# Performance work log

Measured on AMD Instinct MI355X. Metric: run time of the kernel, lower is better.

The kernel has to match this reference:

```python
import jax, jax.numpy as jnp
import numpy as np

B, E, H, N = 16, 1024, 16, 2048
Eh = E // H   # head dim = 64
BH = B * H    # 256


def setup_inputs() -> dict:
    key = jax.random.key(0)
    ks = jax.random.split(key, 12)
    query = jax.random.normal(ks[0], (B, E), jnp.float32)
    key_in = jax.random.normal(ks[1], (B, E), jnp.float32)
    value = jax.random.normal(ks[2], (B, E), jnp.float32)
    # State as it would look in steady state: a_sum ~ O(N) positive,
    # q_mem stores already-scaled queries (small), k/v unit-ish scale.
    a_sum_mem = float(N) * (0.9 + 0.2 * jax.random.uniform(ks[3], (BH, N - 1), jnp.float32))
    av_mem = (0.1 * float(N)) * jax.random.normal(ks[4], (BH, N - 1, Eh), jnp.float32)
    q_mem = 0.06 * jax.random.normal(ks[5], (BH, N, Eh), jnp.float32)
    k_t_mem = 0.5 * jax.random.normal(ks[6], (BH, Eh, N), jnp.float32)
    v_mem = 0.5 * jax.random.normal(ks[7], (BH, N, Eh), jnp.float32)
    in_proj_weight = 0.02 * jax.random.normal(ks[8], (3 * E, E), jnp.float32)
    in_proj_bias = jnp.zeros((3 * E,), jnp.float32)
    out_proj_weight = 0.02 * jax.random.normal(ks[9], (E, E), jnp.float32)
    out_proj_bias = jnp.zeros((E,), jnp.float32)
    return dict(query=query, key=key_in, value=value,
                a_sum_mem=a_sum_mem, av_mem=av_mem, q_mem=q_mem,
                k_t_mem=k_t_mem, v_mem=v_mem,
                in_proj_weight=in_proj_weight, in_proj_bias=in_proj_bias,
                out_proj_weight=out_proj_weight, out_proj_bias=out_proj_bias)


def _sdpa_step(a_sum_mem, av_mem, q_mem, k_t_mem, v_mem, q_step, k_step, v_step):
    # Faithful port of _scaled_dot_product_attention_step.
    q_step = q_step / jnp.sqrt(jnp.float32(Eh))          # (BH, Eh)
    q_old = q_mem[:, 0]                                   # (BH, Eh)
    k_old = k_t_mem[:, :, 0]                              # (BH, Eh)
    q_sel = jnp.stack((q_old, q_step), axis=1)            # (BH, 2, Eh)
    k_sel = jnp.stack((k_old, k_step), axis=2)            # (BH, Eh, 2)
    a_tb = jnp.exp(jnp.einsum('bte,bes->bts', q_sel, k_t_mem[:, :, 1:]))  # (BH, 2, N-1)
    a_lr = jnp.exp(jnp.einsum('bne,bet->bnt', q_mem[:, 1:, :], k_sel))    # (BH, N-1, 2)
    a_br = jnp.exp(jnp.sum(q_step * k_step, axis=1))      # (BH,)
    a_sum = jnp.concatenate(
        [a_sum_mem + a_lr[:, :, 1] - a_lr[:, :, 0],
         (a_tb[:, 1].sum(axis=1) + a_br)[:, None]], axis=1)               # (BH, N)
    av_top = (av_mem
              - a_lr[:, :, 0, None] * v_mem[:, 0][:, None, :]
              + a_lr[:, :, 1, None] * v_step[:, None, :])                 # (BH, N-1, Eh)
    av_bot = jnp.einsum('bs,bse->be', a_tb[:, 1], v_mem[:, 1:]) + a_br[:, None] * v_step
    av = jnp.concatenate([av_top, av_bot[:, None, :]], axis=1)            # (BH, N, Eh)
    out = av / a_sum[..., None]
    new_state = (a_sum[:, 1:], av[:, 1:],
                 jnp.concatenate([q_mem[:, 1:], q_step[:, None, :]], axis=1),
                 jnp.concatenate([k_t_mem[:, :, 1:], k_step[:, :, None]], axis=2),
                 jnp.concatenate([v_mem[:, 1:], v_step[:, None, :]], axis=1))
    return out, new_state


def reference(query, key, value, a_sum_mem, av_mem, q_mem, k_t_mem, v_mem,
              in_proj_weight, in_proj_bias, out_proj_weight, out_proj_bias):
    # Packed in-projection (q/k/v chunks of the packed weight).
    w_q, w_k, w_v = jnp.split(in_proj_weight, 3, axis=0)
    b_q, b_k, b_v = jnp.split(in_proj_bias, 3)
    q = (query @ w_q.T + b_q).reshape(BH, Eh)   # head split: (B, H*Eh) -> (B*H, Eh)
    k = (key @ w_k.T + b_k).reshape(BH, Eh)
    v = (value @ w_v.T + b_v).reshape(BH, Eh)
    attn, new_state = _sdpa_step(a_sum_mem, av_mem, q_mem, k_t_mem, v_mem, q, k, v)
    # (BH, N, Eh) -> (N, BH, Eh) -> (N, B, E), then output projection.
    attn = attn.transpose(1, 0, 2).reshape(N, B, E)
    out = attn @ out_proj_weight.T + out_proj_bias    # (N, B, E)
    return (out,) + new_state
```

## Files before the change

kernel.cpp:

```cpp
#include <hip/hip_runtime.h>
#include <hip/hip_bf16.h>

constexpr int kB  = 16;
constexpr int kE  = 1024;
constexpr int kH  = 16;
constexpr int kN  = 2048;
constexpr int kEh = 64;
constexpr int kBH = 256;
constexpr int kM  = kN * kB;

typedef __bf16 bf16x8 __attribute__((ext_vector_type(8)));
typedef float  f32x4  __attribute__((ext_vector_type(4)));

static __device__ __forceinline__ unsigned short bf16_bits(float f) {
  union { __hip_bfloat16 h; unsigned short u; } cv;
  cv.h = __float2bfloat16(f);
  return cv.u;
}

__global__ __launch_bounds__(256) void proj_kernel(
    const float* __restrict__ query, const float* __restrict__ key_in,
    const float* __restrict__ value, const float* __restrict__ W,
    const float* __restrict__ bias,
    float* __restrict__ q_step, float* __restrict__ k_step,
    float* __restrict__ v_step) {
  int j   = blockIdx.x;
  int mat = j >> 10;
  int col = j & 1023;
  const float* in = (mat == 0) ? query : ((mat == 1) ? key_in : value);
  const float* wrow = W + (size_t)j * kE;
  int tid = threadIdx.x;

  float4 w4 = reinterpret_cast<const float4*>(wrow)[tid];
  float part[16];
#pragma unroll
  for (int r = 0; r < 16; ++r) {
    float4 in4 = reinterpret_cast<const float4*>(in + (size_t)r * kE)[tid];
    part[r] = w4.x * in4.x + w4.y * in4.y + w4.z * in4.z + w4.w * in4.w;
  }
#pragma unroll
  for (int r = 0; r < 16; ++r) {
    float v = part[r];
    for (int off = 32; off > 0; off >>= 1) v += __shfl_down(v, off, 64);
    part[r] = v;
  }
  __shared__ float red[4][16];
  int wave = threadIdx.x >> 6;
  int lane = threadIdx.x & 63;
  if (lane == 0) {
#pragma unroll
    for (int r = 0; r < 16; ++r) red[wave][r] = part[r];
  }
  __syncthreads();
  if (threadIdx.x < 16) {
    int r = threadIdx.x;
    float v = red[0][r] + red[1][r] + red[2][r] + red[3][r] + bias[j];
    int h = col >> 6, eh = col & 63;
    int bh = r * kH + h;
    if (mat == 0)      q_step[bh * kEh + eh] = v * 0.125f;
    else if (mat == 1) k_step[bh * kEh + eh] = v;
    else               v_step[bh * kEh + eh] = v;
  }
}

__global__ void wcvt_kernel(const float* __restrict__ w,
                            __hip_bfloat16* __restrict__ o, int n) {
  int i = blockIdx.x * blockDim.x + threadIdx.x;
  if (i < n) o[i] = __float2bfloat16(w[i]);
}

__global__ __launch_bounds__(256) void kt_kernel(
    const float* __restrict__ k_t_mem, const float* __restrict__ q_step,
    float* __restrict__ k_t_out, float* __restrict__ a_tb1,
    float* __restrict__ top_sum) {
  int b = blockIdx.x;
  int chunk = blockIdx.y;
  __shared__ float qs[64];
  if (threadIdx.x < 64) qs[threadIdx.x] = q_step[b * kEh + threadIdx.x];
  __syncthreads();

  int c4 = (chunk * 256 + threadIdx.x) * 4;
  bool last = (c4 + 4 >= kN);
  const float* src = k_t_mem + (size_t)b * kEh * kN;
  float* dst = k_t_out + (size_t)b * kEh * kN;

  f32x4 dot = {0.f, 0.f, 0.f, 0.f};
#pragma unroll 4
  for (int e = 0; e < 64; ++e) {
    float4 a = reinterpret_cast<const float4*>(src + (size_t)e * kN)[c4 >> 2];
    float s3 = last ? 0.f : src[(size_t)e * kN + c4 + 4];
    float4 sh = {a.y, a.z, a.w, s3};
    reinterpret_cast<float4*>(dst + (size_t)e * kN)[c4 >> 2] = sh;
    float q = qs[e];
    dot.x += q * sh.x;
    dot.y += q * sh.y;
    dot.z += q * sh.z;
    dot.w += q * sh.w;
  }
  float tx = __expf(dot.x);
  float ty = __expf(dot.y);
  float tz = __expf(dot.z);
  float tw = last ? 0.f : __expf(dot.w);

  float* tbrow = a_tb1 + (size_t)b * (kN - 1);
  tbrow[c4 + 0] = tx;
  tbrow[c4 + 1] = ty;
  tbrow[c4 + 2] = tz;
  if (!last) tbrow[c4 + 3] = tw;

  float s = tx + ty + tz + tw;
  for (int off = 32; off > 0; off >>= 1) s += __shfl_xor(s, off, 64);
  __shared__ float red[4];
  int wave = threadIdx.x >> 6, lane = threadIdx.x & 63;
  if (lane == 0) red[wave] = s;
  __syncthreads();
  if (threadIdx.x == 0)
    atomicAdd(&top_sum[b], red[0] + red[1] + red[2] + red[3]);
}

__global__ __launch_bounds__(256) void qav_kernel(
    const float* __restrict__ q_mem, const float* __restrict__ av_mem,
    const float* __restrict__ a_sum_mem, const float* __restrict__ k_t_mem,
    const float* __restrict__ v_mem, const float* __restrict__ k_step,
    const float* __restrict__ v_step, float* __restrict__ q_out,
    float* __restrict__ av_out, float* __restrict__ a_sum_out,
    __hip_bfloat16* __restrict__ attn) {
  int b = blockIdx.x;
  int chunk = blockIdx.y;
  int wave = threadIdx.x >> 6, lane = threadIdx.x & 63;
  int g = lane >> 4, c = lane & 15;
  int b_ = b >> 4, h = b & 15;

  float4 kst  = reinterpret_cast<const float4*>(k_step + (size_t)b * kEh)[c];
  float4 vst  = reinterpret_cast<const float4*>(v_step + (size_t)b * kEh)[c];
  float4 vold = reinterpret_cast<const float4*>(v_mem + (size_t)b * kN * kEh)[c];
  const float* kt0 = k_t_mem + (size_t)b * kEh * kN;
  float4 kold;
  kold.x = kt0[(size_t)(4 * c + 0) * kN];
  kold.y = kt0[(size_t)(4 * c + 1) * kN];
  kold.z = kt0[(size_t)(4 * c + 2) * kN];
  kold.w = kt0[(size_t)(4 * c + 3) * kN];

  unsigned short* attn_u = reinterpret_cast<unsigned short*>(attn);

  int jb = chunk * 64 + wave * 16;
#pragma unroll
  for (int it = 0; it < 4; ++it) {
    int j = jb + it * 4 + g;
    bool valid = (j <= kN - 2);
    int jc = valid ? j : (kN - 2);

    float4 q4 = reinterpret_cast<const float4*>(
        q_mem + ((size_t)b * kN + (jc + 1)) * kEh)[c];
    float p0 = q4.x * kold.x + q4.y * kold.y + q4.z * kold.z + q4.w * kold.w;
    float p1 = q4.x * kst.x + q4.y * kst.y + q4.z * kst.z + q4.w * kst.w;
#pragma unroll
    for (int off = 1; off < 16; off <<= 1) {
      p0 += __shfl_xor(p0, off, 64);
      p1 += __shfl_xor(p1, off, 64);
    }
    float a0 = __expf(p0);
    float a1 = __expf(p1);
    float asum = a_sum_mem[(size_t)b * (kN - 1) + jc] + a1 - a0;
    float4 av4 = reinterpret_cast<const float4*>(
        av_mem + ((size_t)b * (kN - 1) + jc) * kEh)[c];
    float4 avv;
    avv.x = av4.x - a0 * vold.x + a1 * vst.x;
    avv.y = av4.y - a0 * vold.y + a1 * vst.y;
    avv.z = av4.z - a0 * vold.z + a1 * vst.z;
    avv.w = av4.w - a0 * vold.w + a1 * vst.w;

    if (valid) {
      reinterpret_cast<float4*>(q_out + ((size_t)b * kN + jc) * kEh)[c] = q4;
      float inv = 1.0f / asum;
      ushort4 pk;
      pk.x = bf16_bits(avv.x * inv);
      pk.y = bf16_bits(avv.y * inv);
      pk.z = bf16_bits(avv.z * inv);
      pk.w = bf16_bits(avv.w * inv);
      *reinterpret_cast<ushort4*>(
          attn_u + ((size_t)jc * kB + b_) * kE + h * kEh + c * 4) = pk;
      if (j >= 1) {
        reinterpret_cast<float4*>(
            av_out + ((size_t)b * (kN - 1) + (jc - 1)) * kEh)[c] = avv;
        if (c == 0) a_sum_out[(size_t)b * (kN - 1) + (jc - 1)] = asum;
      }
    }
  }
}

__global__ __launch_bounds__(256) void v_kernel(
    const float* __restrict__ v_mem, const float* __restrict__ a_tb1,
    float* __restrict__ v_out, float* __restrict__ av_last) {
  int b = blockIdx.x;
  int chunk = blockIdx.y;
  int wave = threadIdx.x >> 6, lane = threadIdx.x & 63;
  int g = lane >> 4, c = lane & 15;
  const float* vsrc = v_mem + (size_t)b * kN * kEh;
  float* vdst = v_out + (size_t)b * kN * kEh;
  const float* tb = a_tb1 + (size_t)b * (kN - 1);

  f32x4 acc = {0.f, 0.f, 0.f, 0.f};
  int sbase = chunk * 256 + wave * 64;
#pragma unroll 4
  for (int it = 0; it < 16; ++it) {
    int s = sbase + it * 4 + g;
    bool valid = (s <= kN - 2);
    int sc = valid ? s : (kN - 2);
    float t = valid ? tb[sc] : 0.f;
    float4 vv = reinterpret_cast<const float4*>(vsrc + (size_t)(sc + 1) * kEh)[c];
    acc.x += t * vv.x;
    acc.y += t * vv.y;
    acc.z += t * vv.z;
    acc.w += t * vv.w;
    if (valid)
      reinterpret_cast<float4*>(vdst + (size_t)sc * kEh)[c] = vv;
  }
#pragma unroll
  for (int off = 16; off <= 32; off <<= 1) {
    acc.x += __shfl_xor(acc.x, off, 64);
    acc.y += __shfl_xor(acc.y, off, 64);
    acc.z += __shfl_xor(acc.z, off, 64);
    acc.w += __shfl_xor(acc.w, off, 64);
  }
  __shared__ f32x4 red[4][16];
  if (g == 0) red[wave][c] = acc;
  __syncthreads();
  if (threadIdx.x < 16) {
    f32x4 a0 = red[0][threadIdx.x], a1 = red[1][threadIdx.x];
    f32x4 a2 = red[2][threadIdx.x], a3 = red[3][threadIdx.x];
    float* dst = av_last + (size_t)b * kEh + threadIdx.x * 4;
    atomicAdd(dst + 0, a0.x + a1.x + a2.x + a3.x);
    atomicAdd(dst + 1, a0.y + a1.y + a2.y + a3.y);
    atomicAdd(dst + 2, a0.z + a1.z + a2.z + a3.z);
    atomicAdd(dst + 3, a0.w + a1.w + a2.w + a3.w);
  }
}

__global__ __launch_bounds__(64) void final_kernel(
    const float* __restrict__ q_step, const float* __restrict__ k_step,
    const float* __restrict__ v_step, const float* __restrict__ top_sum,
    const float* __restrict__ av_last_in, float* __restrict__ q_out,
    float* __restrict__ k_t_out, float* __restrict__ v_out,
    float* __restrict__ a_sum_out, float* __restrict__ av_out,
    __hip_bfloat16* __restrict__ attn) {
  int b = blockIdx.x;
  int lane = threadIdx.x;
  int b_ = b >> 4, h = b & 15;
  float qs = q_step[b * kEh + lane];
  float ks = k_step[b * kEh + lane];
  float vs = v_step[b * kEh + lane];
  float p = qs * ks;
  for (int off = 32; off > 0; off >>= 1) p += __shfl_xor(p, off, 64);
  float abr = __expf(p);
  float asum = top_sum[b] + abr;
  float avl = av_last_in[b * kEh + lane] + abr * vs;
  attn[((size_t)(kN - 1) * kB + b_) * kE + h * kEh + lane] =
      __float2bfloat16(avl / asum);
  if (lane == 0) a_sum_out[(size_t)b * (kN - 1) + (kN - 2)] = asum;
  av_out[((size_t)b * (kN - 1) + (kN - 2)) * kEh + lane] = avl;
  q_out[((size_t)b * kN + (kN - 1)) * kEh + lane] = qs;
  k_t_out[(size_t)b * kEh * kN + (size_t)lane * kN + (kN - 1)] = ks;
  v_out[((size_t)b * kN + (kN - 1)) * kEh + lane] = vs;
}

#define BM 128
#define BN 128
#define BK 64

__global__ __launch_bounds__(256) void gemm_kernel(
    const __bf16* __restrict__ A, const __bf16* __restrict__ Bw,
    const float* __restrict__ bias, float* __restrict__ C,
    int M, int Ncols, int K) {
  __shared__ __bf16 lA[BM * BK];
  __shared__ __bf16 lB[BN * BK];
  int tid = threadIdx.x;
  int m0 = blockIdx.x * BM;
  int n0 = blockIdx.y * BN;
  int wave = tid >> 6;
  int lane = tid & 63;
  int wm = (wave & 1) * 64;
  int wn = (wave >> 1) * 64;

  f32x4 zero = {0.f, 0.f, 0.f, 0.f};
  f32x4 acc[4][4];
#pragma unroll
  for (int i = 0; i < 4; ++i)
#pragma unroll
    for (int j = 0; j < 4; ++j) acc[i][j] = zero;

  int quad = lane >> 4;
  int mrow = lane & 15;

  for (int k0 = 0; k0 < K; k0 += BK) {
#pragma unroll
    for (int r = 0; r < 4; ++r) {
      int off = r * 4096 + tid * 16;
      int row = off >> 7;
      int col8 = (off >> 4) & 7;
      const __bf16* ga = A + ((size_t)(m0 + row) * K + k0 + col8 * 8);
      const __bf16* gb = Bw + ((size_t)(n0 + row) * K + k0 + col8 * 8);
      __builtin_amdgcn_global_load_lds(
          (const __attribute__((address_space(1))) void*)ga,
          (__attribute__((address_space(3))) void*)((char*)lA + off), 16, 0, 0);
      __builtin_amdgcn_global_load_lds(
          (const __attribute__((address_space(1))) void*)gb,
          (__attribute__((address_space(3))) void*)((char*)lB + off), 16, 0, 0);
    }
    __syncthreads();

#pragma unroll
    for (int kk = 0; kk < 2; ++kk) {
      bf16x8 af[4], bfr[4];
#pragma unroll
      for (int i = 0; i < 4; ++i) {
        af[i]  = *(const bf16x8*)(&lA[(wm + i * 16 + mrow) * BK + kk * 32 + quad * 8]);
        bfr[i] = *(const bf16x8*)(&lB[(wn + i * 16 + mrow) * BK + kk * 32 + quad * 8]);
      }
#pragma unroll
      for (int i = 0; i < 4; ++i)
#pragma unroll
        for (int j = 0; j < 4; ++j)
          acc[i][j] = __builtin_amdgcn_mfma_f32_16x16x32_bf16(
              af[i], bfr[j], acc[i][j], 0, 0, 0);
    }
    __syncthreads();
  }

  int colq = lane & 15;
  int rowq = lane >> 4;
#pragma unroll
  for (int i = 0; i < 4; ++i) {
#pragma unroll
    for (int j = 0; j < 4; ++j) {
      int col = n0 + wn + j * 16 + colq;
      float bv = bias[col];
      size_t base = (size_t)(m0 + wm + i * 16 + rowq * 4) * Ncols + col;
#pragma unroll
      for (int r = 0; r < 4; ++r) {
        C[base + (size_t)r * Ncols] = acc[i][j][r] + bv;
      }
    }
  }
}

extern "C" void kernel_launch(void* const* d_in, const int* in_sizes, int n_in,
                              void* d_out, int out_size, void* d_ws,
                              size_t ws_size, hipStream_t stream) {
  const float* query          = (const float*)d_in[0];
  const float* key_in         = (const float*)d_in[1];
  const float* value          = (const float*)d_in[2];
  const float* a_sum_mem      = (const float*)d_in[3];
  const float* av_mem         = (const float*)d_in[4];
  const float* q_mem          = (const float*)d_in[5];
  const float* k_t_mem        = (const float*)d_in[6];
  const float* v_mem          = (const float*)d_in[7];
  const float* in_proj_weight = (const float*)d_in[8];
  const float* in_proj_bias   = (const float*)d_in[9];
  const float* out_proj_weight= (const float*)d_in[10];
  const float* out_proj_bias  = (const float*)d_in[11];

  float* out       = (float*)d_out;
  float* a_sum_out = out + (size_t)kN * kB * kE;
  float* av_out    = a_sum_out + (size_t)kBH * (kN - 1);
  float* q_out     = av_out + (size_t)kBH * (kN - 1) * kEh;
  float* k_t_out   = q_out + (size_t)kBH * kN * kEh;
  float* v_out     = k_t_out + (size_t)kBH * kEh * kN;

  char* ws = (char*)d_ws;
  float* q_step  = (float*)ws;
  float* k_step  = q_step + 16384;
  float* v_step  = k_step + 16384;
  float* top_sum = v_step + 16384;
  float* av_last = top_sum + 256;
  float* a_tb1   = av_last + 16384;
  __hip_bfloat16* wo_bf   = (__hip_bfloat16*)(ws + 2359296);
  __hip_bfloat16* attn_bf = (__hip_bfloat16*)(ws + 4456448);

  hipMemsetAsync(ws + 196608, 0, 66560, stream);

  proj_kernel<<<3 * kE, 256, 0, stream>>>(query, key_in, value, in_proj_weight,
                                          in_proj_bias, q_step, k_step, v_step);
  wcvt_kernel<<<(kE * kE) / 256, 256, 0, stream>>>(out_proj_weight, wo_bf,
                                                   kE * kE);
  kt_kernel<<<dim3(kBH, 2), 256, 0, stream>>>(k_t_mem, q_step, k_t_out, a_tb1,
                                              top_sum);
  qav_kernel<<<dim3(kBH, 32), 256, 0, stream>>>(q_mem, av_mem, a_sum_mem,
                                                k_t_mem, v_mem, k_step, v_step,
                                                q_out, av_out, a_sum_out,
                                                attn_bf);
  v_kernel<<<dim3(kBH, 8), 256, 0, stream>>>(v_mem, a_tb1, v_out, av_last);
  final_kernel<<<kBH, 64, 0, stream>>>(q_step, k_step, v_step, top_sum,
                                       av_last, q_out, k_t_out, v_out,
                                       a_sum_out, av_out, attn_bf);
  gemm_kernel<<<dim3(kM / BM, kE / BN), 256, 0, stream>>>(
      (const __bf16*)attn_bf, (const __bf16*)wo_bf, out_proj_bias, out, kM, kE,
      kE);
}
```

Before: 1.172 ms.

## Merge streaming kernels into one launch with nontemporal memory ops

Folds the weight-conversion kernel into the projection kernel as extra blocks. Merges the k_t shift, q/av update and v shift kernels into a single streaming kernel. The top-row exp weights now stay in shared memory instead of a global scratch buffer, and each k_t/v block covers 1024 columns. Nontemporal loads and stores are applied to the large streaming buffers and to the GEMM output, to cut launch count and cache pollution. The cost is fewer, larger k_t/v blocks with longer serial loops, which may lower parallelism for that part.

```diff
diff --git a/kernel.cpp b/kernel.cpp
--- a/kernel.cpp
+++ b/kernel.cpp
@@ -11,6 +11,7 @@
 
 typedef __bf16 bf16x8 __attribute__((ext_vector_type(8)));
 typedef float  f32x4  __attribute__((ext_vector_type(4)));
+typedef unsigned short u16x4 __attribute__((ext_vector_type(4)));
 
 static __device__ __forceinline__ unsigned short bf16_bits(float f) {
   union { __hip_bfloat16 h; unsigned short u; } cv;
@@ -18,18 +19,37 @@
   return cv.u;
 }
 
-__global__ __launch_bounds__(256) void proj_kernel(
+static __device__ __forceinline__ f32x4 nt_load4(const float* p) {
+  return __builtin_nontemporal_load(reinterpret_cast<const f32x4*>(p));
+}
+static __device__ __forceinline__ void nt_store4(float* p, f32x4 v) {
+  __builtin_nontemporal_store(v, reinterpret_cast<f32x4*>(p));
+}
+
+__global__ __launch_bounds__(256) void prep_kernel(
     const float* __restrict__ query, const float* __restrict__ key_in,
     const float* __restrict__ value, const float* __restrict__ W,
     const float* __restrict__ bias,
     float* __restrict__ q_step, float* __restrict__ k_step,
-    float* __restrict__ v_step) {
-  int j   = blockIdx.x;
+    float* __restrict__ v_step,
+    const float* __restrict__ wo, __hip_bfloat16* __restrict__ wo_bf) {
+  __shared__ float red[4][16];
+  int bid = blockIdx.x;
+  int tid = threadIdx.x;
+  if (bid >= 3072) {
+    int i4 = ((bid - 3072) * 256 + tid) * 4;
+    f32x4 w4 = nt_load4(wo + i4);
+    u16x4 o;
+    o[0] = bf16_bits(w4[0]); o[1] = bf16_bits(w4[1]);
+    o[2] = bf16_bits(w4[2]); o[3] = bf16_bits(w4[3]);
+    *reinterpret_cast<u16x4*>(reinterpret_cast<unsigned short*>(wo_bf) + i4) = o;
+    return;
+  }
+  int j   = bid;
   int mat = j >> 10;
   int col = j & 1023;
   const float* in = (mat == 0) ? query : ((mat == 1) ? key_in : value);
   const float* wrow = W + (size_t)j * kE;
-  int tid = threadIdx.x;
 
   float4 w4 = reinterpret_cast<const float4*>(wrow)[tid];
   float part[16];
@@ -44,16 +64,15 @@
     for (int off = 32; off > 0; off >>= 1) v += __shfl_down(v, off, 64);
     part[r] = v;
   }
-  __shared__ float red[4][16];
-  int wave = threadIdx.x >> 6;
-  int lane = threadIdx.x & 63;
+  int wave = tid >> 6;
+  int lane = tid & 63;
   if (lane == 0) {
 #pragma unroll
     for (int r = 0; r < 16; ++r) red[wave][r] = part[r];
   }
   __syncthreads();
-  if (threadIdx.x < 16) {
-    int r = threadIdx.x;
+  if (tid < 16) {
+    int r = tid;
     float v = red[0][r] + red[1][r] + red[2][r] + red[3][r] + bias[j];
     int h = col >> 6, eh = col & 63;
     int bh = r * kH + h;
@@ -63,23 +82,93 @@
   }
 }
 
-__global__ void wcvt_kernel(const float* __restrict__ w,
-                            __hip_bfloat16* __restrict__ o, int n) {
-  int i = blockIdx.x * blockDim.x + threadIdx.x;
-  if (i < n) o[i] = __float2bfloat16(w[i]);
-}
-
-__global__ __launch_bounds__(256) void kt_kernel(
-    const float* __restrict__ k_t_mem, const float* __restrict__ q_step,
-    float* __restrict__ k_t_out, float* __restrict__ a_tb1,
-    float* __restrict__ top_sum) {
-  int b = blockIdx.x;
-  int chunk = blockIdx.y;
+__global__ __launch_bounds__(256) void stream_kernel(
+    const float* __restrict__ q_mem, const float* __restrict__ av_mem,
+    const float* __restrict__ a_sum_mem, const float* __restrict__ k_t_mem,
+    const float* __restrict__ v_mem, const float* __restrict__ q_step,
+    const float* __restrict__ k_step, const float* __restrict__ v_step,
+    float* __restrict__ q_out, float* __restrict__ av_out,
+    float* __restrict__ a_sum_out, float* __restrict__ k_t_out,
+    float* __restrict__ v_out, float* __restrict__ top_sum,
+    float* __restrict__ av_last, __hip_bfloat16* __restrict__ attn) {
   __shared__ float qs[64];
-  if (threadIdx.x < 64) qs[threadIdx.x] = q_step[b * kEh + threadIdx.x];
+  __shared__ float tbuf[1024];
+  __shared__ f32x4 redv[4][16];
+  __shared__ float redt[4];
+
+  int bid = blockIdx.x;
+  int tid = threadIdx.x;
+  int wave = tid >> 6, lane = tid & 63;
+
+  if (bid < 8192) {
+    int b = bid >> 5;
+    int chunk = bid & 31;
+    int g = lane >> 4, c = lane & 15;
+    int b_ = b >> 4, h = b & 15;
+
+    f32x4 kst  = *reinterpret_cast<const f32x4*>(k_step + (size_t)b * kEh + c * 4);
+    f32x4 vst  = *reinterpret_cast<const f32x4*>(v_step + (size_t)b * kEh + c * 4);
+    f32x4 vold = *reinterpret_cast<const f32x4*>(v_mem + (size_t)b * kN * kEh + c * 4);
+    const float* kt0 = k_t_mem + (size_t)b * kEh * kN;
+    f32x4 kold;
+    kold[0] = kt0[(size_t)(4 * c + 0) * kN];
+    kold[1] = kt0[(size_t)(4 * c + 1) * kN];
+    kold[2] = kt0[(size_t)(4 * c + 2) * kN];
+    kold[3] = kt0[(size_t)(4 * c + 3) * kN];
+
+    unsigned short* attn_u = reinterpret_cast<unsigned short*>(attn);
+
+    int jb = chunk * 64 + wave * 16;
+#pragma unroll
+    for (int it = 0; it < 4; ++it) {
+      int j = jb + it * 4 + g;
+      bool valid = (j <= kN - 2);
+      int jc = valid ? j : (kN - 2);
+
+      f32x4 q4 = nt_load4(q_mem + ((size_t)b * kN + (jc + 1)) * kEh + c * 4);
+      float p0 = q4[0] * kold[0] + q4[1] * kold[1] + q4[2] * kold[2] + q4[3] * kold[3];
+      float p1 = q4[0] * kst[0]  + q4[1] * kst[1]  + q4[2] * kst[2]  + q4[3] * kst[3];
+#pragma unroll
+      for (int off = 1; off < 16; off <<= 1) {
+        p0 += __shfl_xor(p0, off, 64);
+        p1 += __shfl_xor(p1, off, 64);
+      }
+      float a0 = __expf(p0);
+      float a1 = __expf(p1);
+      float asum = a_sum_mem[(size_t)b * (kN - 1) + jc] + a1 - a0;
+      f32x4 av4 = nt_load4(av_mem + ((size_t)b * (kN - 1) + jc) * kEh + c * 4);
+      f32x4 avv;
+      avv[0] = av4[0] - a0 * vold[0] + a1 * vst[0];
+      avv[1] = av4[1] - a0 * vold[1] + a1 * vst[1];
+      avv[2] = av4[2] - a0 * vold[2] + a1 * vst[2];
+      avv[3] = av4[3] - a0 * vold[3] + a1 * vst[3];
+
+      if (valid) {
+        nt_store4(q_out + ((size_t)b * kN + jc) * kEh + c * 4, q4);
+        float inv = 1.0f / asum;
+        u16x4 pk;
+        pk[0] = bf16_bits(avv[0] * inv);
+        pk[1] = bf16_bits(avv[1] * inv);
+        pk[2] = bf16_bits(avv[2] * inv);
+        pk[3] = bf16_bits(avv[3] * inv);
+        *reinterpret_cast<u16x4*>(
+            attn_u + ((size_t)jc * kB + b_) * kE + h * kEh + c * 4) = pk;
+        if (j >= 1) {
+          nt_store4(av_out + ((size_t)b * (kN - 1) + (jc - 1)) * kEh + c * 4, avv);
+          if (c == 0) a_sum_out[(size_t)b * (kN - 1) + (jc - 1)] = asum;
+        }
+      }
+    }
+    return;
+  }
+
+  int id2 = bid - 8192;
+  int b = id2 >> 1, chunk = id2 & 1;
+
+  if (tid < 64) qs[tid] = q_step[b * kEh + tid];
   __syncthreads();
 
-  int c4 = (chunk * 256 + threadIdx.x) * 4;
+  int c4 = chunk * 1024 + tid * 4;
   bool last = (c4 + 4 >= kN);
   const float* src = k_t_mem + (size_t)b * kEh * kN;
   float* dst = k_t_out + (size_t)b * kEh * kN;
@@ -87,153 +176,73 @@
   f32x4 dot = {0.f, 0.f, 0.f, 0.f};
 #pragma unroll 4
   for (int e = 0; e < 64; ++e) {
-    float4 a = reinterpret_cast<const float4*>(src + (size_t)e * kN)[c4 >> 2];
-    float s3 = last ? 0.f : src[(size_t)e * kN + c4 + 4];
-    float4 sh = {a.y, a.z, a.w, s3};
-    reinterpret_cast<float4*>(dst + (size_t)e * kN)[c4 >> 2] = sh;
+    f32x4 a = nt_load4(src + (size_t)e * kN + c4);
+    float s3 = last ? 0.f
+                    : __builtin_nontemporal_load(src + (size_t)e * kN + c4 + 4);
+    f32x4 sh;
+    sh[0] = a[1]; sh[1] = a[2]; sh[2] = a[3]; sh[3] = s3;
+    nt_store4(dst + (size_t)e * kN + c4, sh);
     float q = qs[e];
-    dot.x += q * sh.x;
-    dot.y += q * sh.y;
-    dot.z += q * sh.z;
-    dot.w += q * sh.w;
-  }
-  float tx = __expf(dot.x);
-  float ty = __expf(dot.y);
-  float tz = __expf(dot.z);
-  float tw = last ? 0.f : __expf(dot.w);
-
-  float* tbrow = a_tb1 + (size_t)b * (kN - 1);
-  tbrow[c4 + 0] = tx;
-  tbrow[c4 + 1] = ty;
-  tbrow[c4 + 2] = tz;
-  if (!last) tbrow[c4 + 3] = tw;
+    dot[0] += q * sh[0];
+    dot[1] += q * sh[1];
+    dot[2] += q * sh[2];
+    dot[3] += q * sh[3];
+  }
+  float tx = __expf(dot[0]);
+  float ty = __expf(dot[1]);
+  float tz = __expf(dot[2]);
+  float tw = last ? 0.f : __expf(dot[3]);
+
+  tbuf[tid * 4 + 0] = tx;
+  tbuf[tid * 4 + 1] = ty;
+  tbuf[tid * 4 + 2] = tz;
+  tbuf[tid * 4 + 3] = tw;
 
   float s = tx + ty + tz + tw;
   for (int off = 32; off > 0; off >>= 1) s += __shfl_xor(s, off, 64);
-  __shared__ float red[4];
-  int wave = threadIdx.x >> 6, lane = threadIdx.x & 63;
-  if (lane == 0) red[wave] = s;
+  if (lane == 0) redt[wave] = s;
   __syncthreads();
-  if (threadIdx.x == 0)
-    atomicAdd(&top_sum[b], red[0] + red[1] + red[2] + red[3]);
-}
-
-__global__ __launch_bounds__(256) void qav_kernel(
-    const float* __restrict__ q_mem, const float* __restrict__ av_mem,
-    const float* __restrict__ a_sum_mem, const float* __restrict__ k_t_mem,
-    const float* __restrict__ v_mem, const float* __restrict__ k_step,
-    const float* __restrict__ v_step, float* __restrict__ q_out,
-    float* __restrict__ av_out, float* __restrict__ a_sum_out,
-    __hip_bfloat16* __restrict__ attn) {
-  int b = blockIdx.x;
-  int chunk = blockIdx.y;
-  int wave = threadIdx.x >> 6, lane = threadIdx.x & 63;
-  int g = lane >> 4, c = lane & 15;
-  int b_ = b >> 4, h = b & 15;
-
-  float4 kst  = reinterpret_cast<const float4*>(k_step + (size_t)b * kEh)[c];
-  float4 vst  = reinterpret_cast<const float4*>(v_step + (size_t)b * kEh)[c];
-  float4 vold = reinterpret_cast<const float4*>(v_mem + (size_t)b * kN * kEh)[c];
-  const float* kt0 = k_t_mem + (size_t)b * kEh * kN;
-  float4 kold;
-  kold.x = kt0[(size_t)(4 * c + 0) * kN];
-  kold.y = kt0[(size_t)(4 * c + 1) * kN];
-  kold.z = kt0[(size_t)(4 * c + 2) * kN];
-  kold.w = kt0[(size_t)(4 * c + 3) * kN];
-
-  unsigned short* attn_u = reinterpret_cast<unsigned short*>(attn);
-
-  int jb = chunk * 64 + wave * 16;
-#pragma unroll
-  for (int it = 0; it < 4; ++it) {
-    int j = jb + it * 4 + g;
-    bool valid = (j <= kN - 2);
-    int jc = valid ? j : (kN - 2);
-
-    float4 q4 = reinterpret_cast<const float4*>(
-        q_mem + ((size_t)b * kN + (jc + 1)) * kEh)[c];
-    float p0 = q4.x * kold.x + q4.y * kold.y + q4.z * kold.z + q4.w * kold.w;
-    float p1 = q4.x * kst.x + q4.y * kst.y + q4.z * kst.z + q4.w * kst.w;
-#pragma unroll
-    for (int off = 1; off < 16; off <<= 1) {
-      p0 += __shfl_xor(p0, off, 64);
-      p1 += __shfl_xor(p1, off, 64);
-    }
-    float a0 = __expf(p0);
-    float a1 = __expf(p1);
-    float asum = a_sum_mem[(size_t)b * (kN - 1) + jc] + a1 - a0;
-    float4 av4 = reinterpret_cast<const float4*>(
-        av_mem + ((size_t)b * (kN - 1) + jc) * kEh)[c];
-    float4 avv;
-    avv.x = av4.x - a0 * vold.x + a1 * vst.x;
-    avv.y = av4.y - a0 * vold.y + a1 * vst.y;
-    avv.z = av4.z - a0 * vold.z + a1 * vst.z;
-    avv.w = av4.w - a0 * vold.w + a1 * vst.w;
-
-    if (valid) {
-      reinterpret_cast<float4*>(q_out + ((size_t)b * kN + jc) * kEh)[c] = q4;
-      float inv = 1.0f / asum;
-      ushort4 pk;
-      pk.x = bf16_bits(avv.x * inv);
-      pk.y = bf16_bits(avv.y * inv);
-      pk.z = bf16_bits(avv.z * inv);
-      pk.w = bf16_bits(avv.w * inv);
-      *reinterpret_cast<ushort4*>(
-          attn_u + ((size_t)jc * kB + b_) * kE + h * kEh + c * 4) = pk;
-      if (j >= 1) {
-        reinterpret_cast<float4*>(
-            av_out + ((size_t)b * (kN - 1) + (jc - 1)) * kEh)[c] = avv;
-        if (c == 0) a_sum_out[(size_t)b * (kN - 1) + (jc - 1)] = asum;
-      }
-    }
-  }
-}
-
-__global__ __launch_bounds__(256) void v_kernel(
-    const float* __restrict__ v_mem, const float* __restrict__ a_tb1,
-    float* __restrict__ v_out, float* __restrict__ av_last) {
-  int b = blockIdx.x;
-  int chunk = blockIdx.y;
-  int wave = threadIdx.x >> 6, lane = threadIdx.x & 63;
+  if (tid == 0)
+    atomicAdd(&top_sum[b], redt[0] + redt[1] + redt[2] + redt[3]);
+
   int g = lane >> 4, c = lane & 15;
   const float* vsrc = v_mem + (size_t)b * kN * kEh;
   float* vdst = v_out + (size_t)b * kN * kEh;
-  const float* tb = a_tb1 + (size_t)b * (kN - 1);
 
   f32x4 acc = {0.f, 0.f, 0.f, 0.f};
-  int sbase = chunk * 256 + wave * 64;
+  int sbase = chunk * 1024 + wave * 256;
 #pragma unroll 4
-  for (int it = 0; it < 16; ++it) {
-    int s = sbase + it * 4 + g;
-    bool valid = (s <= kN - 2);
-    int sc = valid ? s : (kN - 2);
-    float t = valid ? tb[sc] : 0.f;
-    float4 vv = reinterpret_cast<const float4*>(vsrc + (size_t)(sc + 1) * kEh)[c];
-    acc.x += t * vv.x;
-    acc.y += t * vv.y;
-    acc.z += t * vv.z;
-    acc.w += t * vv.w;
-    if (valid)
-      reinterpret_cast<float4*>(vdst + (size_t)sc * kEh)[c] = vv;
+  for (int it = 0; it < 64; ++it) {
+    int s4 = sbase + it * 4 + g;
+    bool valid = (s4 <= kN - 2);
+    int sc = valid ? s4 : (kN - 2);
+    float t = valid ? tbuf[s4 - chunk * 1024] : 0.f;
+    f32x4 vv = nt_load4(vsrc + (size_t)(sc + 1) * kEh + c * 4);
+    acc[0] += t * vv[0];
+    acc[1] += t * vv[1];
+    acc[2] += t * vv[2];
+    acc[3] += t * vv[3];
+    if (valid) nt_store4(vdst + (size_t)sc * kEh + c * 4, vv);
   }
 #pragma unroll
   for (int off = 16; off <= 32; off <<= 1) {
-    acc.x += __shfl_xor(acc.x, off, 64);
-    acc.y += __shfl_xor(acc.y, off, 64);
-    acc.z += __shfl_xor(acc.z, off, 64);
-    acc.w += __shfl_xor(acc.w, off, 64);
-  }
-  __shared__ f32x4 red[4][16];
-  if (g == 0) red[wave][c] = acc;
+    acc[0] += __shfl_xor(acc[0], off, 64);
+    acc[1] += __shfl_xor(acc[1], off, 64);
+    acc[2] += __shfl_xor(acc[2], off, 64);
+    acc[3] += __shfl_xor(acc[3], off, 64);
+  }
+  if (g == 0) redv[wave][c] = acc;
   __syncthreads();
-  if (threadIdx.x < 16) {
-    f32x4 a0 = red[0][threadIdx.x], a1 = red[1][threadIdx.x];
-    f32x4 a2 = red[2][threadIdx.x], a3 = red[3][threadIdx.x];
-    float* dst = av_last + (size_t)b * kEh + threadIdx.x * 4;
-    atomicAdd(dst + 0, a0.x + a1.x + a2.x + a3.x);
-    atomicAdd(dst + 1, a0.y + a1.y + a2.y + a3.y);
-    atomicAdd(dst + 2, a0.z + a1.z + a2.z + a3.z);
-    atomicAdd(dst + 3, a0.w + a1.w + a2.w + a3.w);
+  if (tid < 16) {
+    f32x4 a0 = redv[0][tid];
+    f32x4 a1 = redv[1][tid];
+    f32x4 a2 = redv[2][tid];
+    f32x4 a3 = redv[3][tid];
+    float* dstl = av_last + (size_t)b * kEh + tid * 4;
+    atomicAdd(dstl + 0, a0[0] + a1[0] + a2[0] + a3[0]);
+    atomicAdd(dstl + 1, a0[1] + a1[1] + a2[1] + a3[1]);
+    atomicAdd(dstl + 2, a0[2] + a1[2] + a2[2] + a3[2]);
+    atomicAdd(dstl + 3, a0[3] + a1[3] + a2[3] + a3[3]);
   }
 }
 
@@ -338,7 +347,8 @@
       size_t base = (size_t)(m0 + wm + i * 16 + rowq * 4) * Ncols + col;
 #pragma unroll
       for (int r = 0; r < 4; ++r) {
-        C[base + (size_t)r * Ncols] = acc[i][j][r] + bv;
+        __builtin_nontemporal_store(acc[i][j][r] + bv,
+                                    &C[base + (size_t)r * Ncols]);
       }
     }
   }
@@ -373,23 +383,18 @@
   float* v_step  = k_step + 16384;
   float* top_sum = v_step + 16384;
   float* av_last = top_sum + 256;
-  float* a_tb1   = av_last + 16384;
   __hip_bfloat16* wo_bf   = (__hip_bfloat16*)(ws + 2359296);
   __hip_bfloat16* attn_bf = (__hip_bfloat16*)(ws + 4456448);
 
   hipMemsetAsync(ws + 196608, 0, 66560, stream);
 
-  proj_kernel<<<3 * kE, 256, 0, stream>>>(query, key_in, value, in_proj_weight,
-                                          in_proj_bias, q_step, k_step, v_step);
-  wcvt_kernel<<<(kE * kE) / 256, 256, 0, stream>>>(out_proj_weight, wo_bf,
-                                                   kE * kE);
-  kt_kernel<<<dim3(kBH, 2), 256, 0, stream>>>(k_t_mem, q_step, k_t_out, a_tb1,
-                                              top_sum);
-  qav_kernel<<<dim3(kBH, 32), 256, 0, stream>>>(q_mem, av_mem, a_sum_mem,
-                                                k_t_mem, v_mem, k_step, v_step,
-                                                q_out, av_out, a_sum_out,
-                                                attn_bf);
-  v_kernel<<<dim3(kBH, 8), 256, 0, stream>>>(v_mem, a_tb1, v_out, av_last);
+  prep_kernel<<<4096, 256, 0, stream>>>(query, key_in, value, in_proj_weight,
+                                        in_proj_bias, q_step, k_step, v_step,
+                                        out_proj_weight, wo_bf);
+  stream_kernel<<<8704, 256, 0, stream>>>(q_mem, av_mem, a_sum_mem, k_t_mem,
+                                          v_mem, q_step, k_step, v_step, q_out,
+                                          av_out, a_sum_out, k_t_out, v_out,
+                                          top_sum, av_last, attn_bf);
   final_kernel<<<kBH, 64, 0, stream>>>(q_step, k_step, v_step, top_sum,
                                        av_last, q_out, k_t_out, v_out,
                                        a_sum_out, av_out, attn_bf);
```

Result: faster. 1.138 ms (-2.9%).
